# Optimization experiments

Hardware: AMD Instinct MI355X
Metric: run time of the kernel (lower is better)

## Reference

```python
import jax, jax.numpy as jnp
import numpy as np

NUM_HEADS = 8
MASK_NEG = -1e30


def setup_inputs() -> dict:
    key = jax.random.key(0)
    k1, k2, k3 = jax.random.split(key, 3)
    B, S, D = 8, 2048, 128
    queries = jax.random.normal(k1, (B, S, D), dtype=jnp.float32)
    mask = jnp.ones((B, S), dtype=jnp.float32)
    # kernel_size=1 Conv1D with no bias == dense matmul over last dim
    W_q = jax.random.normal(k2, (D, D), dtype=jnp.float32) * (D ** -0.5)
    W_mem = jax.random.normal(k3, (D, 2 * D), dtype=jnp.float32) * (D ** -0.5)
    return {"queries": queries, "mask": mask, "W_q": W_q, "W_mem": W_mem}


def _split_heads(x, h):
    # [B, S, D] -> [B, h, S, D/h]
    B, S, D = x.shape
    return x.reshape(B, S, h, D // h).transpose(0, 2, 1, 3)


def reference(queries, mask, W_q, W_mem):
    B, S, D = queries.shape
    h = NUM_HEADS
    scale = (D // h) ** -0.5
    memory = jnp.einsum('bsd,de->bse', queries, W_mem)   # [B,S,2D]
    query = jnp.einsum('bsd,de->bse', queries, W_q)      # [B,S,D]
    K, V = jnp.split(memory, 2, axis=2)
    Q = _split_heads(query, h) * scale                   # [B,h,S,dh]
    K = _split_heads(K, h)
    V = _split_heads(V, h)
    logits = jnp.einsum('bhqd,bhkd->bhqk', Q, K)         # [B,h,S,S]
    m = mask.reshape(B, 1, 1, S)
    logits = logits + (1.0 - m) * MASK_NEG
    weights = jax.nn.softmax(logits, axis=-1)
    # dropout is identity at inference (training=None)
    x = jnp.einsum('bhqk,bhkd->bhqd', weights, V)        # [B,h,S,dh]
    return x.transpose(0, 2, 1, 3).reshape(B, S, D)
```

## Files before the change

### kernel.cpp

```cpp
#include <hip/hip_runtime.h>
#include <hip/hip_bf16.h>
#include <stdint.h>

#define B_    8
#define S_    2048
#define D_    128
#define H_    8
#define DH_   16
#define BH_   64
#define E_    384
#define NT_   (S_ / 32)

typedef __attribute__((ext_vector_type(4)))  short short4v;
typedef __attribute__((ext_vector_type(8)))  short short8;
typedef __attribute__((ext_vector_type(4)))  float f32x4;
typedef __attribute__((ext_vector_type(16))) float f32x16;

__device__ inline unsigned short f2b(float f) {
    union { __bf16 h; unsigned short u; } t;
    t.h = (__bf16)f;
    return t.u;
}
__device__ inline float b2f(unsigned short u) {
    union { unsigned u; float f; } x; x.u = ((unsigned)u) << 16; return x.f;
}
__device__ inline int dperm(int d) {
    return (d & 3) | ((d & 8) >> 1) | ((d & 4) << 1);
}

__device__ inline void gload_lds16(const void* g, void* l) {
    __builtin_amdgcn_global_load_lds(
        (const __attribute__((address_space(1))) unsigned int*)g,
        (__attribute__((address_space(3))) unsigned int*)l, 16, 0, 0);
}

#define EXPB 16250.7346f

__global__ void wtrans_kernel(const float* __restrict__ Wq,
                              const float* __restrict__ Wmem,
                              unsigned short* __restrict__ wt) {
    int e = blockIdx.x, k = threadIdx.x;
    float v = (e < 128) ? Wq[k * 128 + e] : Wmem[k * 256 + (e - 128)];
    wt[e * 128 + k] = f2b(v);
}

__global__ __launch_bounds__(512) void proj_kernel(
        const float* __restrict__ X, const float* __restrict__ mask,
        const unsigned short* __restrict__ wt,
        unsigned short* __restrict__ Qb, unsigned short* __restrict__ Kf,
        unsigned short* __restrict__ Vf) {
    __shared__ unsigned short Xs[64][136];
    __shared__ unsigned short Vs[64][136];
    __shared__ float Ms[64];
    const int tid = threadIdx.x;
    const int b = blockIdx.x & 7, st = blockIdx.x >> 3;
    const int s0 = st * 64;
    const float* Xp = X + ((size_t)b * S_ + s0) * D_;

    for (int i = tid; i < 64 * D_ / 4; i += 512) {
        f32x4 v = __builtin_nontemporal_load((const f32x4*)Xp + i);
        int row = i >> 5, c4 = (i & 31) * 4;
        Xs[row][c4 + 0] = f2b(v[0]); Xs[row][c4 + 1] = f2b(v[1]);
        Xs[row][c4 + 2] = f2b(v[2]); Xs[row][c4 + 3] = f2b(v[3]);
    }
    if (tid < 64) Ms[tid] = mask[(size_t)b * S_ + s0 + tid];
    __syncthreads();

    const int wid = tid >> 6, lane = tid & 63;
    const int lr = lane & 15, lg = lane >> 4;
    const float qscale = 0.25f * 1.44269504088896f;

    for (int ci = 0; ci < 3; ++ci) {
        const int ct = wid + ci * 8;
        const int e0 = ct * 16;
        short4v bfr[8];
        #pragma unroll
        for (int kk = 0; kk < 8; ++kk)
            bfr[kk] = *(const short4v*)&wt[(e0 + lr) * 128 + kk * 16 + lg * 4];
        for (int rt = 0; rt < 4; ++rt) {
            f32x4 acc; acc[0] = acc[1] = acc[2] = acc[3] = 0.f;
            #pragma unroll
            for (int kk = 0; kk < 8; ++kk) {
                short4v a = *(const short4v*)&Xs[rt * 16 + lr][kk * 16 + lg * 4];
                acc = __builtin_amdgcn_mfma_f32_16x16x16bf16_1k(a, bfr[kk], acc, 0, 0, 0);
            }
            const int e = e0 + lr;
            #pragma unroll
            for (int r = 0; r < 4; ++r) {
                const int sl = rt * 16 + lg * 4 + r;
                const float v = acc[r];
                if (e < 128) {
                    int hh = e >> 4, d = dperm(e & 15);
                    Qb[(((size_t)b * H_ + hh) * S_ + s0 + sl) * DH_ + d] = f2b(v * qscale);
                } else if (e < 256) {
                    int ek = e - 128, hh = ek >> 4, d = dperm(ek & 15);
                    int T = st * 2 + (sl >> 5), qq = sl & 31;
                    int l = qq + 32 * (d >> 3), j = d & 7;
                    Kf[(((size_t)(b * H_ + hh) * NT_ + T) * 64 + l) * 8 + j] = f2b(v);
                } else {
                    Vs[sl][e - 256] = f2b(v);
                }
            }
        }
    }
    __syncthreads();

    for (int j = tid; j < H_ * 2 * 2 * 64; j += 512) {
        const int l = j & 63, f = (j >> 6) & 1, t = (j >> 7) & 1, hh = j >> 8;
        const int q = l & 31, h = l >> 5;
        const int vrow = (q < 16) ? q : 16;
        const int T = st * 2 + t;
        unsigned short* dst =
            Vf + ((((size_t)(b * H_ + hh) * NT_ + T) * 2 + f) * 64 + l) * 8;
        union { unsigned short us[8]; short8 v; } o;
        #pragma unroll
        for (int e = 0; e < 8; ++e) {
            const int p = f * 16 + 8 * h + e;
            const int sl = (p & 16) | dperm(p & 15);
            const int srow = t * 32 + sl;
            const float mk = Ms[srow];
            o.us[e] = f2b((vrow == 16) ? mk : b2f(Vs[srow][hh * 16 + vrow]) * mk);
        }
        *(short8*)dst = o.v;
    }
}

__global__ __launch_bounds__(512, 4) void attn_kernel(
        const unsigned short* __restrict__ Qb, const unsigned short* __restrict__ Kf,
        const unsigned short* __restrict__ Vf, float* __restrict__ out) {
    const int tid = threadIdx.x;
    const int wid = tid >> 6, lane = tid & 63;
    const int q = lane & 31, h = lane >> 5;
    const int p = blockIdx.x;
    const int bh = (p & 7) * 8 + ((p >> 3) & 7);
    const int qt = p >> 6;
    const int q0 = qt * 128 + (wid >> 1) * 32;
    const int hf = wid & 1;

    __shared__ unsigned short ldsKV[4][6][64][8];

    const unsigned short* ksrc = Kf + (size_t)bh * S_ * DH_;
    const unsigned short* vsrc = Vf + (size_t)bh * NT_ * 1024;

    const short8 qf = *(const short8*)&Qb[((size_t)bh * S_ + q0 + q) * DH_ + 8 * h];

    f32x16 acc, z;
    #pragma unroll
    for (int i = 0; i < 16; ++i) { acc[i] = 0.f; z[i] = 0.f; }

    const int s_h3 = wid / 3, s_s = wid % 3;

#define STAGE(JS_)                                                             \
    if (wid < 6) {                                                             \
        const int js_ = (JS_);                                                 \
        const int tt_ = s_h3 * 32 + js_;                                       \
        const unsigned short* gp_ =                                            \
            (s_s == 0) ? ksrc + (size_t)tt_ * 512 + lane * 8                   \
                       : vsrc + (size_t)tt_ * 1024 + (s_s - 1) * 512 + lane * 8;\
        gload_lds16(gp_, &ldsKV[js_ & 3][wid][0][0]);                          \
    }

    STAGE(0); STAGE(1); STAGE(2); STAGE(3);

    for (int j = 0; j < 32; ++j) {
        asm volatile("s_waitcnt vmcnt(3)" ::: "memory");
        __builtin_amdgcn_s_barrier();
        asm volatile("" ::: "memory");

        const int slot = j & 3;
        const short8 kf  = *(const short8*)&ldsKV[slot][3 * hf + 0][lane][0];
        const short8 va0 = *(const short8*)&ldsKV[slot][3 * hf + 1][lane][0];
        const short8 va1 = *(const short8*)&ldsKV[slot][3 * hf + 2][lane][0];

        asm volatile("s_waitcnt lgkmcnt(0)" ::: "memory");
        __builtin_amdgcn_s_barrier();
        asm volatile("" ::: "memory");

        STAGE((j + 4) & 31);

        __builtin_amdgcn_s_setprio(1);
        f32x16 s0 = __builtin_amdgcn_mfma_f32_32x32x16_bf16(kf, qf, z, 0, 0, 0);
        __builtin_amdgcn_s_setprio(0);

        union { unsigned u[4]; short8 v; } b0, b1;
        #pragma unroll
        for (int i = 0; i < 4; ++i) {
            const int l0 = (int)__builtin_fmaf(s0[2 * i],     128.f, EXPB);
            const int h0 = (int)__builtin_fmaf(s0[2 * i + 1], 128.f, EXPB);
            b0.u[i] = (unsigned)l0 | ((unsigned)h0 << 16);
            const int l1 = (int)__builtin_fmaf(s0[8 + 2 * i],     128.f, EXPB);
            const int h1 = (int)__builtin_fmaf(s0[8 + 2 * i + 1], 128.f, EXPB);
            b1.u[i] = (unsigned)l1 | ((unsigned)h1 << 16);
        }
        __builtin_amdgcn_s_setprio(1);
        acc = __builtin_amdgcn_mfma_f32_32x32x16_bf16(va0, b0.v, acc, 0, 0, 0);
        acc = __builtin_amdgcn_mfma_f32_32x32x16_bf16(va1, b1.v, acc, 0, 0, 0);
        __builtin_amdgcn_s_setprio(0);
    }
#undef STAGE

    asm volatile("s_waitcnt vmcnt(0)" ::: "memory");
    __syncthreads();

    float (*cmb)[16][64] = (float (*)[16][64]) & ldsKV[0][0][0][0];
    if (wid & 1) {
        #pragma unroll
        for (int i = 0; i < 16; ++i)
            cmb[wid >> 1][i][lane] = acc[i];
    }
    __syncthreads();
    if (!(wid & 1)) {
        const int b = bh >> 3, head = bh & 7;
        float* obase = out + ((size_t)b * S_ + q0 + q) * D_ + head * DH_ + 4 * h;
        float o[16];
        #pragma unroll
        for (int i = 0; i < 16; ++i) o[i] = acc[i] + cmb[wid >> 1][i][lane];
        const float r = 1.0f / o[8];
        *(float4*)obase       = make_float4(o[0] * r, o[1] * r, o[2] * r, o[3] * r);
        *(float4*)(obase + 8) = make_float4(o[4] * r, o[5] * r, o[6] * r, o[7] * r);
    }
}

extern "C" void kernel_launch(void* const* d_in, const int* in_sizes, int n_in,
                              void* d_out, int out_size, void* d_ws, size_t ws_size,
                              hipStream_t stream) {
    const float* X    = (const float*)d_in[0];
    const float* mask = (const float*)d_in[1];
    const float* Wq   = (const float*)d_in[2];
    const float* Wmem = (const float*)d_in[3];
    float* out = (float*)d_out;

    unsigned short* Qb = (unsigned short*)d_ws;
    unsigned short* Kf = Qb + (size_t)BH_ * S_ * DH_;
    unsigned short* Vf = Kf + (size_t)BH_ * S_ * DH_;
    unsigned short* wt = Vf + (size_t)BH_ * NT_ * 2 * 64 * 8;

    wtrans_kernel<<<E_, 128, 0, stream>>>(Wq, Wmem, wt);
    proj_kernel<<<B_ * S_ / 64, 512, 0, stream>>>(X, mask, wt, Qb, Kf, Vf);
    attn_kernel<<<BH_ * (S_ / 128), 512, 0, stream>>>(Qb, Kf, Vf, out);
}
```

Before: 62.31 us.

## Interleave K/V tiles and give each wave its own LDS pipeline without barriers

K and V fragments for each 32-key tile are packed together into one interleaved KV buffer. Each wave now stages its own tiles into a private double-buffered LDS region, so the workgroup-wide barriers inside the attention loop can be dropped. The occupancy hint rises to 6 blocks per EU. Waves that share key tiles now each load their own copy, which adds global and LDS traffic, and the deeper prefetch ring becomes double buffering.

```diff
diff --git a/kernel.cpp b/kernel.cpp
--- a/kernel.cpp
+++ b/kernel.cpp
@@ -47,8 +47,7 @@
 __global__ __launch_bounds__(512) void proj_kernel(
         const float* __restrict__ X, const float* __restrict__ mask,
         const unsigned short* __restrict__ wt,
-        unsigned short* __restrict__ Qb, unsigned short* __restrict__ Kf,
-        unsigned short* __restrict__ Vf) {
+        unsigned short* __restrict__ Qb, unsigned short* __restrict__ KVf) {
     __shared__ unsigned short Xs[64][136];
     __shared__ unsigned short Vs[64][136];
     __shared__ float Ms[64];
@@ -96,7 +95,7 @@
                     int ek = e - 128, hh = ek >> 4, d = dperm(ek & 15);
                     int T = st * 2 + (sl >> 5), qq = sl & 31;
                     int l = qq + 32 * (d >> 3), j = d & 7;
-                    Kf[(((size_t)(b * H_ + hh) * NT_ + T) * 64 + l) * 8 + j] = f2b(v);
+                    KVf[((size_t)(b * H_ + hh) * NT_ + T) * 1536 + l * 8 + j] = f2b(v);
                 } else {
                     Vs[sl][e - 256] = f2b(v);
                 }
@@ -111,7 +110,7 @@
         const int vrow = (q < 16) ? q : 16;
         const int T = st * 2 + t;
         unsigned short* dst =
-            Vf + ((((size_t)(b * H_ + hh) * NT_ + T) * 2 + f) * 64 + l) * 8;
+            KVf + ((size_t)(b * H_ + hh) * NT_ + T) * 1536 + (1 + f) * 512 + l * 8;
         union { unsigned short us[8]; short8 v; } o;
         #pragma unroll
         for (int e = 0; e < 8; ++e) {
@@ -125,9 +124,9 @@
     }
 }
 
-__global__ __launch_bounds__(512, 4) void attn_kernel(
-        const unsigned short* __restrict__ Qb, const unsigned short* __restrict__ Kf,
-        const unsigned short* __restrict__ Vf, float* __restrict__ out) {
+__global__ __launch_bounds__(512, 6) void attn_kernel(
+        const unsigned short* __restrict__ Qb, const unsigned short* __restrict__ KVf,
+        float* __restrict__ out) {
     const int tid = threadIdx.x;
     const int wid = tid >> 6, lane = tid & 63;
     const int q = lane & 31, h = lane >> 5;
@@ -135,12 +134,12 @@
     const int bh = (p & 7) * 8 + ((p >> 3) & 7);
     const int qt = p >> 6;
     const int q0 = qt * 128 + (wid >> 1) * 32;
-    const int hf = wid & 1;
-
-    __shared__ unsigned short ldsKV[4][6][64][8];
-
-    const unsigned short* ksrc = Kf + (size_t)bh * S_ * DH_;
-    const unsigned short* vsrc = Vf + (size_t)bh * NT_ * 1024;
+    const int ttBase = (wid & 1) * (NT_ / 2);
+    const int ttEnd  = ttBase + NT_ / 2;
+
+    __shared__ unsigned short lds[8][2][3][64][8];
+
+    const unsigned short* kv = KVf + (size_t)bh * NT_ * 1536 + (size_t)lane * 8;
 
     const short8 qf = *(const short8*)&Qb[((size_t)bh * S_ + q0 + q) * DH_ + 8 * h];
 
@@ -148,35 +147,28 @@
     #pragma unroll
     for (int i = 0; i < 16; ++i) { acc[i] = 0.f; z[i] = 0.f; }
 
-    const int s_h3 = wid / 3, s_s = wid % 3;
-
-#define STAGE(JS_)                                                             \
-    if (wid < 6) {                                                             \
-        const int js_ = (JS_);                                                 \
-        const int tt_ = s_h3 * 32 + js_;                                       \
-        const unsigned short* gp_ =                                            \
-            (s_s == 0) ? ksrc + (size_t)tt_ * 512 + lane * 8                   \
-                       : vsrc + (size_t)tt_ * 1024 + (s_s - 1) * 512 + lane * 8;\
-        gload_lds16(gp_, &ldsKV[js_ & 3][wid][0][0]);                          \
-    }
-
-    STAGE(0); STAGE(1); STAGE(2); STAGE(3);
-
+#define STAGE(TT_, SL_)                                                        \
+    {                                                                          \
+        const unsigned short* g_ = kv + (size_t)(TT_) * 1536;                  \
+        gload_lds16(g_,        &lds[wid][SL_][0][0][0]);                       \
+        gload_lds16(g_ + 512,  &lds[wid][SL_][1][0][0]);                       \
+        gload_lds16(g_ + 1024, &lds[wid][SL_][2][0][0]);                       \
+    }
+
+    STAGE(ttBase, 0); STAGE(ttBase + 1, 1);
+
+    #pragma unroll 2
     for (int j = 0; j < 32; ++j) {
+        const int slot = j & 1;
         asm volatile("s_waitcnt vmcnt(3)" ::: "memory");
-        __builtin_amdgcn_s_barrier();
-        asm volatile("" ::: "memory");
-
-        const int slot = j & 3;
-        const short8 kf  = *(const short8*)&ldsKV[slot][3 * hf + 0][lane][0];
-        const short8 va0 = *(const short8*)&ldsKV[slot][3 * hf + 1][lane][0];
-        const short8 va1 = *(const short8*)&ldsKV[slot][3 * hf + 2][lane][0];
-
+        __builtin_amdgcn_sched_barrier(0);
+        const short8 kf  = *(const short8*)&lds[wid][slot][0][lane][0];
+        const short8 va0 = *(const short8*)&lds[wid][slot][1][lane][0];
+        const short8 va1 = *(const short8*)&lds[wid][slot][2][lane][0];
         asm volatile("s_waitcnt lgkmcnt(0)" ::: "memory");
-        __builtin_amdgcn_s_barrier();
-        asm volatile("" ::: "memory");
-
-        STAGE((j + 4) & 31);
+        __builtin_amdgcn_sched_barrier(0);
+        const int nt2 = ttBase + j + 2;
+        STAGE(nt2 < ttEnd ? nt2 : nt2 - 32, slot);
 
         __builtin_amdgcn_s_setprio(1);
         f32x16 s0 = __builtin_amdgcn_mfma_f32_32x32x16_bf16(kf, qf, z, 0, 0, 0);
@@ -202,7 +194,7 @@
     asm volatile("s_waitcnt vmcnt(0)" ::: "memory");
     __syncthreads();
 
-    float (*cmb)[16][64] = (float (*)[16][64]) & ldsKV[0][0][0][0];
+    float (*cmb)[16][64] = (float (*)[16][64]) & lds[0][0][0][0][0];
     if (wid & 1) {
         #pragma unroll
         for (int i = 0; i < 16; ++i)
@@ -230,12 +222,11 @@
     const float* Wmem = (const float*)d_in[3];
     float* out = (float*)d_out;
 
-    unsigned short* Qb = (unsigned short*)d_ws;
-    unsigned short* Kf = Qb + (size_t)BH_ * S_ * DH_;
-    unsigned short* Vf = Kf + (size_t)BH_ * S_ * DH_;
-    unsigned short* wt = Vf + (size_t)BH_ * NT_ * 2 * 64 * 8;
+    unsigned short* Qb  = (unsigned short*)d_ws;
+    unsigned short* KVf = Qb + (size_t)BH_ * S_ * DH_;
+    unsigned short* wt  = KVf + (size_t)BH_ * NT_ * 1536;
 
     wtrans_kernel<<<E_, 128, 0, stream>>>(Wq, Wmem, wt);
-    proj_kernel<<<B_ * S_ / 64, 512, 0, stream>>>(X, mask, wt, Qb, Kf, Vf);
-    attn_kernel<<<BH_ * (S_ / 128), 512, 0, stream>>>(Qb, Kf, Vf, out);
-}
+    proj_kernel<<<B_ * S_ / 64, 512, 0, stream>>>(X, mask, wt, Qb, KVf);
+    attn_kernel<<<BH_ * (S_ / 128), 512, 0, stream>>>(Qb, KVf, out);
+}
```

After: 63.84 us. 1.02x slower.
